# Kernel optimization log

Hardware: AMD Instinct MI355X
Metric: run time of the kernel (lower is better)

Reference implementation:

```python
import jax, jax.numpy as jnp
import numpy as np

B, S, N, H, V = 8, 512, 32, 256, 100001
NEG = -1e9
SLOPE = 0.2  # LeakyReLU negative slope


def setup_inputs() -> dict:
    key = jax.random.key(0)
    k1, k2, k3, k4, k5 = jax.random.split(key, 5)
    node_ids = jax.random.randint(k1, (B, S), 0, V)
    neighs = jax.random.randint(k2, (B, S, N), 0, V)
    mask = jax.random.randint(k3, (B, S, N, 1), 0, 2).astype(jnp.int32)
    emb_table = jax.random.normal(k4, (V, H), dtype=jnp.float32) * 0.02
    a_w = jax.random.normal(k5, (2 * H, 1), dtype=jnp.float32) * (1.0 / np.sqrt(2 * H))
    a_b = jnp.zeros((1,), dtype=jnp.float32)
    return {"node_ids": node_ids, "neighs": neighs, "mask": mask,
            "emb_table": emb_table, "a_w": a_w, "a_b": a_b}


def reference(node_ids, neighs, mask, emb_table, a_w, a_b):
    # Gather embeddings
    src = emb_table[node_ids][:, :, None, :]          # [B,S,1,H]
    nbr = emb_table[neighs]                           # [B,S,N,H]
    neigh_embs = jnp.concatenate([src, nbr], axis=2)  # [B,S,N+1,H] (self + neighbors)
    # Concat src with each candidate -> [B,S,N+1,2H]
    src_rep = jnp.broadcast_to(src, neigh_embs.shape)
    embs = jnp.concatenate([src_rep, neigh_embs], axis=-1)
    # Tiny linear (2H -> 1) + LeakyReLU(0.2)
    z = embs @ a_w + a_b                              # [B,S,N+1,1]
    att = jnp.where(z > 0, z, SLOPE * z)
    # Mask neighbor slots (self at index 0 is never masked)
    att = att.at[:, :, 1:].add(mask.astype(att.dtype) * NEG)
    w = jax.nn.softmax(att, axis=2)                   # [B,S,N+1,1]
    # Weighted aggregate: w^T @ neigh_embs
    out = jnp.sum(w * neigh_embs, axis=2)             # [B,S,H]
    return out
```

## Files before the change

### kernel.cpp

```cpp
#include <hip/hip_runtime.h>
#include <math.h>


constexpr int H  = 256;
constexpr int NN = 32;
constexpr int C  = NN + 1;
constexpr int PF = 8;
constexpr float SLOPE = 0.2f;
constexpr float NEGV  = -1e9f;

__device__ __forceinline__ float wave_sum(float v) {
#pragma unroll
  for (int off = 32; off > 0; off >>= 1)
    v += __shfl_xor(v, off, 64);
  return v;
}

__global__ __launch_bounds__(256, 4) void gat_kernel(
    const int*   __restrict__ node_ids,
    const int*   __restrict__ neighs,
    const int*   __restrict__ mask,
    const float* __restrict__ emb,
    const float* __restrict__ a_w,
    const float* __restrict__ a_b,
    float*       __restrict__ out,
    int npos)
{
  const int wid  = (blockIdx.x * blockDim.x + threadIdx.x) >> 6;
  const int lane = threadIdx.x & 63;
  if (wid >= npos) return;
  const int l4 = lane << 2;

  const float4 aw1 = *(const float4*)(a_w + l4);
  const float4 aw2 = *(const float4*)(a_w + H + l4);
  const float  ab  = a_b[0];

  int   my_idx  = 0;
  float my_madd = 0.f;
  if (lane == 0) {
    my_idx = node_ids[wid];
  } else if (lane <= NN) {
    my_idx  = neighs[wid * NN + lane - 1];
    my_madd = mask[wid * NN + lane - 1] ? NEGV : 0.f;
  }

  const float4* __restrict__ embv = (const float4*)emb;

  auto row_lane = [&](int c) -> float4 {
    int ic = __builtin_amdgcn_readfirstlane(__shfl(my_idx, c, 64));
    return embv[(size_t)ic * (H / 4) + lane];
  };

  float4 buf[PF];
#pragma unroll
  for (int i = 0; i < PF; ++i) buf[i] = row_lane(i);

  float  m = -1e30f, s = 0.f;
  float  zsrc = 0.f;
  float4 acc = {0.f, 0.f, 0.f, 0.f};

#pragma unroll
  for (int c = 0; c < C; ++c) {
    const float4 cur = buf[c & (PF - 1)];
    if (c + PF < C) buf[c & (PF - 1)] = row_lane(c + PF);

    float p = cur.x * aw2.x + cur.y * aw2.y + cur.z * aw2.z + cur.w * aw2.w;
    if (c == 0) {
      float ps = cur.x * aw1.x + cur.y * aw1.y + cur.z * aw1.z + cur.w * aw1.w;
      zsrc = wave_sum(ps);
    }
    float z = zsrc + wave_sum(p) + ab;
    float a = (z > 0.f) ? z : SLOPE * z;
    a += __shfl(my_madd, c, 64);

    const float mnew  = fmaxf(m, a);
    const float scale = __expf(m - mnew);
    const float pr    = __expf(a - mnew);
    s = s * scale + pr;
    acc.x = acc.x * scale + pr * cur.x;
    acc.y = acc.y * scale + pr * cur.y;
    acc.z = acc.z * scale + pr * cur.z;
    acc.w = acc.w * scale + pr * cur.w;
    m = mnew;
  }

  const float inv = 1.f / s;
  float4 o = {acc.x * inv, acc.y * inv, acc.z * inv, acc.w * inv};
  *(float4*)(out + (size_t)wid * H + l4) = o;
}

extern "C" void kernel_launch(void* const* d_in, const int* in_sizes, int n_in,
                              void* d_out, int out_size, void* d_ws, size_t ws_size,
                              hipStream_t stream) {
  const int*   node_ids = (const int*)d_in[0];
  const int*   neighs   = (const int*)d_in[1];
  const int*   mask     = (const int*)d_in[2];
  const float* emb      = (const float*)d_in[3];
  const float* a_w      = (const float*)d_in[4];
  const float* a_b      = (const float*)d_in[5];
  float*       out      = (float*)d_out;

  const int npos = in_sizes[0];
  const int waves_per_block = 256 / 64;
  const int grid = (npos + waves_per_block - 1) / waves_per_block;

  gat_kernel<<<grid, 256, 0, stream>>>(node_ids, neighs, mask, emb, a_w, a_b,
                                       out, npos);
}
```

Baseline: 158.4 us.

## Precompute per-row attention projections and do a two-pass softmax before aggregation

A new kernel streams the whole embedding table once per call and computes both halves of the attention dot product for every row, storing them in workspace. The gather kernel then gets each candidate's score with a scalar load, does one wave-wide max/sum softmax across lanes, and its aggregation loop becomes plain weighted FMAs. This replaces the online softmax and its per-candidate wave reductions. In exchange it adds a full pass over the table, which is larger than the rows actually gathered, plus an extra launch and workspace use.

After: 176.0 us. 11.1% more time.

```diff
diff --git a/kernel.cpp b/kernel.cpp
--- a/kernel.cpp
+++ b/kernel.cpp
@@ -16,12 +16,45 @@
   return v;
 }
 
+__device__ __forceinline__ float wave_max(float v) {
+#pragma unroll
+  for (int off = 32; off > 0; off >>= 1)
+    v = fmaxf(v, __shfl_xor(v, off, 64));
+  return v;
+}
+
+__device__ __forceinline__ float lane_bcast(float v, int lane) {
+  return __uint_as_float(__builtin_amdgcn_readlane(__float_as_uint(v), lane));
+}
+
+__global__ __launch_bounds__(256, 8) void proj_kernel(
+    const float* __restrict__ emb,
+    const float* __restrict__ a_w,
+    float* __restrict__ h,
+    float* __restrict__ g,
+    int V)
+{
+  const int row  = (blockIdx.x * blockDim.x + threadIdx.x) >> 6;
+  const int lane = threadIdx.x & 63;
+  if (row >= V) return;
+  const int l4 = lane << 2;
+  const float4 e  = *(const float4*)(emb + (size_t)row * H + l4);
+  const float4 w1 = *(const float4*)(a_w + l4);
+  const float4 w2 = *(const float4*)(a_w + H + l4);
+  float p1 = e.x * w1.x + e.y * w1.y + e.z * w1.z + e.w * w1.w;
+  float p2 = e.x * w2.x + e.y * w2.y + e.z * w2.z + e.w * w2.w;
+  p1 = wave_sum(p1);
+  p2 = wave_sum(p2);
+  if (lane == 0) { h[row] = p1; g[row] = p2; }
+}
+
 __global__ __launch_bounds__(256, 4) void gat_kernel(
     const int*   __restrict__ node_ids,
     const int*   __restrict__ neighs,
     const int*   __restrict__ mask,
     const float* __restrict__ emb,
-    const float* __restrict__ a_w,
+    const float* __restrict__ h,
+    const float* __restrict__ g,
     const float* __restrict__ a_b,
     float*       __restrict__ out,
     int npos)
@@ -30,10 +63,6 @@
   const int lane = threadIdx.x & 63;
   if (wid >= npos) return;
   const int l4 = lane << 2;
-
-  const float4 aw1 = *(const float4*)(a_w + l4);
-  const float4 aw2 = *(const float4*)(a_w + H + l4);
-  const float  ab  = a_b[0];
 
   int   my_idx  = 0;
   float my_madd = 0.f;
@@ -44,10 +73,22 @@
     my_madd = mask[wid * NN + lane - 1] ? NEGV : 0.f;
   }
 
+  float gv = (lane <= NN) ? g[my_idx] : 0.f;
+  float hv = (lane == 0)  ? h[my_idx] : 0.f;
+  const float hs = lane_bcast(hv, 0);
+  const float z  = hs + gv + a_b[0];
+  float a = (z > 0.f) ? z : SLOPE * z;
+  a += my_madd;
+  if (lane > NN) a = -1e30f;
+
+  const float m  = wave_max(a);
+  const float p  = __expf(a - m);
+  const float sm = wave_sum(p);
+  const float w  = p * (1.f / sm);
+
   const float4* __restrict__ embv = (const float4*)emb;
-
   auto row_lane = [&](int c) -> float4 {
-    int ic = __builtin_amdgcn_readfirstlane(__shfl(my_idx, c, 64));
+    const int ic = __builtin_amdgcn_readlane(my_idx, c);
     return embv[(size_t)ic * (H / 4) + lane];
   };
 
@@ -55,38 +96,18 @@
 #pragma unroll
   for (int i = 0; i < PF; ++i) buf[i] = row_lane(i);
 
-  float  m = -1e30f, s = 0.f;
-  float  zsrc = 0.f;
   float4 acc = {0.f, 0.f, 0.f, 0.f};
-
 #pragma unroll
   for (int c = 0; c < C; ++c) {
     const float4 cur = buf[c & (PF - 1)];
     if (c + PF < C) buf[c & (PF - 1)] = row_lane(c + PF);
-
-    float p = cur.x * aw2.x + cur.y * aw2.y + cur.z * aw2.z + cur.w * aw2.w;
-    if (c == 0) {
-      float ps = cur.x * aw1.x + cur.y * aw1.y + cur.z * aw1.z + cur.w * aw1.w;
-      zsrc = wave_sum(ps);
-    }
-    float z = zsrc + wave_sum(p) + ab;
-    float a = (z > 0.f) ? z : SLOPE * z;
-    a += __shfl(my_madd, c, 64);
-
-    const float mnew  = fmaxf(m, a);
-    const float scale = __expf(m - mnew);
-    const float pr    = __expf(a - mnew);
-    s = s * scale + pr;
-    acc.x = acc.x * scale + pr * cur.x;
-    acc.y = acc.y * scale + pr * cur.y;
-    acc.z = acc.z * scale + pr * cur.z;
-    acc.w = acc.w * scale + pr * cur.w;
-    m = mnew;
+    const float wc = lane_bcast(w, c);
+    acc.x += wc * cur.x;
+    acc.y += wc * cur.y;
+    acc.z += wc * cur.z;
+    acc.w += wc * cur.w;
   }
-
-  const float inv = 1.f / s;
-  float4 o = {acc.x * inv, acc.y * inv, acc.z * inv, acc.w * inv};
-  *(float4*)(out + (size_t)wid * H + l4) = o;
+  *(float4*)(out + (size_t)wid * H + l4) = acc;
 }
 
 extern "C" void kernel_launch(void* const* d_in, const int* in_sizes, int n_in,
@@ -101,9 +122,21 @@
   float*       out      = (float*)d_out;
 
   const int npos = in_sizes[0];
-  const int waves_per_block = 256 / 64;
-  const int grid = (npos + waves_per_block - 1) / waves_per_block;
+  const int V    = in_sizes[3] / H;
+  const int Vpad = (V + 255) & ~255;
 
-  gat_kernel<<<grid, 256, 0, stream>>>(node_ids, neighs, mask, emb, a_w, a_b,
-                                       out, npos);
+  float* hbuf = (float*)d_ws;
+  float* gbuf = hbuf + Vpad;
+
+  {
+    const int waves_per_block = 256 / 64;
+    const int grid = (V + waves_per_block - 1) / waves_per_block;
+    proj_kernel<<<grid, 256, 0, stream>>>(emb, a_w, hbuf, gbuf, V);
+  }
+  {
+    const int waves_per_block = 256 / 64;
+    const int grid = (npos + waves_per_block - 1) / waves_per_block;
+    gat_kernel<<<grid, 256, 0, stream>>>(node_ids, neighs, mask, emb,
+                                         hbuf, gbuf, a_b, out, npos);
+  }
 }
```

## Compact unmasked candidates via ballot and skip gathers for masked neighbors

Applied to the files above, without the earlier changes.

Uses a wave ballot to compact the indices of unmasked candidates (self plus neighbors whose mask is zero) into shared memory. The online-softmax loop then runs only over those K candidates. Embedding rows whose softmax weight would underflow to zero are no longer gathered. This trades fixed unrolled control flow for a data-dependent trip count, plus a small LDS write/read per wave.

Result: slower. 183.4 us (+15.8%).

```diff
diff --git a/kernel.cpp b/kernel.cpp
--- a/kernel.cpp
+++ b/kernel.cpp
@@ -7,7 +7,6 @@
 constexpr int C  = NN + 1;
 constexpr int PF = 8;
 constexpr float SLOPE = 0.2f;
-constexpr float NEGV  = -1e9f;
 
 __device__ __forceinline__ float wave_sum(float v) {
 #pragma unroll
@@ -26,7 +25,10 @@
     float*       __restrict__ out,
     int npos)
 {
+  __shared__ int slds[4][C + 7];
+
   const int wid  = (blockIdx.x * blockDim.x + threadIdx.x) >> 6;
+  const int wv   = (threadIdx.x >> 6);
   const int lane = threadIdx.x & 63;
   if (wid >= npos) return;
   const int l4 = lane << 2;
@@ -35,44 +37,50 @@
   const float4 aw2 = *(const float4*)(a_w + H + l4);
   const float  ab  = a_b[0];
 
-  int   my_idx  = 0;
-  float my_madd = 0.f;
+  bool active = false;
+  int  my_idx = 0;
   if (lane == 0) {
     my_idx = node_ids[wid];
+    active = true;
   } else if (lane <= NN) {
-    my_idx  = neighs[wid * NN + lane - 1];
-    my_madd = mask[wid * NN + lane - 1] ? NEGV : 0.f;
+    my_idx = neighs[wid * NN + lane - 1];
+    active = (mask[wid * NN + lane - 1] == 0);
+  }
+
+  const unsigned long long bal = __ballot(active);
+  const int K = __popcll(bal);
+  if (active) {
+    const int rank = __popcll(bal & ((1ull << lane) - 1ull));
+    slds[wv][rank] = my_idx;
   }
 
   const float4* __restrict__ embv = (const float4*)emb;
-
-  auto row_lane = [&](int c) -> float4 {
-    int ic = __builtin_amdgcn_readfirstlane(__shfl(my_idx, c, 64));
+  auto row = [&](int k) -> float4 {
+    const int ic = __builtin_amdgcn_readfirstlane(slds[wv][k]);
     return embv[(size_t)ic * (H / 4) + lane];
   };
 
   float4 buf[PF];
 #pragma unroll
-  for (int i = 0; i < PF; ++i) buf[i] = row_lane(i);
+  for (int i = 0; i < PF; ++i)
+    if (i < K) buf[i] = row(i);
 
-  float  m = -1e30f, s = 0.f;
-  float  zsrc = 0.f;
+  float  m = -1e30f, s = 0.f, zsrc = 0.f;
   float4 acc = {0.f, 0.f, 0.f, 0.f};
 
 #pragma unroll
   for (int c = 0; c < C; ++c) {
+    if (c >= K) break;
     const float4 cur = buf[c & (PF - 1)];
-    if (c + PF < C) buf[c & (PF - 1)] = row_lane(c + PF);
+    if (c + PF < K) buf[c & (PF - 1)] = row(c + PF);
 
     float p = cur.x * aw2.x + cur.y * aw2.y + cur.z * aw2.z + cur.w * aw2.w;
     if (c == 0) {
       float ps = cur.x * aw1.x + cur.y * aw1.y + cur.z * aw1.z + cur.w * aw1.w;
       zsrc = wave_sum(ps);
     }
-    float z = zsrc + wave_sum(p) + ab;
-    float a = (z > 0.f) ? z : SLOPE * z;
-    a += __shfl(my_madd, c, 64);
-
+    const float z = zsrc + wave_sum(p) + ab;
+    const float a = (z > 0.f) ? z : SLOPE * z;
     const float mnew  = fmaxf(m, a);
     const float scale = __expf(m - mnew);
     const float pr    = __expf(a - mnew);
```
